# Kernel optimization log

Hardware: AMD Instinct MI355X
Metric: run time of the kernel (lower is better)

Reference implementation:

```python
import jax, jax.numpy as jnp
import numpy as np

N = 65536      # H*W pixels (256x256)
S = 1024       # superpixels
C = 128        # input channels
HIDE = 128     # hidden width
OUT = 64       # per-branch width (hide//2, concat=True)
CLS = 16       # classes
E_A = 16384    # superpixel adjacency edges
E_IMP = 6144   # importance (k=6) edges
E_PX = 1048576 # pixel row/col mask edges
EPS = 1e-5


def setup_inputs() -> dict:
    key = jax.random.key(0)
    ks = iter(jax.random.split(key, 64))
    nrm = lambda shape: jax.random.normal(next(ks), shape, dtype=jnp.float32) * 0.05
    uni = lambda shape, lo=0.0, hi=1.0: jax.random.uniform(next(ks), shape, dtype=jnp.float32, minval=lo, maxval=hi)
    ridx = lambda shape, hi: jax.random.randint(next(ks), shape, 0, hi, dtype=jnp.int32)
    d = {}
    d['x'] = jax.random.normal(next(ks), (N, C), dtype=jnp.float32)
    d['Q'] = uni((N, S))
    d['prelin_w'] = nrm((C, HIDE)); d['prelin_b'] = jnp.zeros((HIDE,), jnp.float32)
    d['bn0_g'] = jnp.ones((HIDE,), jnp.float32); d['bn0_b'] = jnp.zeros((HIDE,), jnp.float32)
    d['bn0_m'] = nrm((HIDE,)); d['bn0_v'] = uni((HIDE,), 0.5, 1.5)
    d['mmpn_w'] = nrm((5, HIDE, HIDE)); d['mmpn_b'] = jnp.zeros((5, HIDE), jnp.float32)
    d['mmpn_bn_g'] = jnp.ones((5, HIDE), jnp.float32); d['mmpn_bn_b'] = jnp.zeros((5, HIDE), jnp.float32)
    d['mmpn_bn_m'] = nrm((5, HIDE)); d['mmpn_bn_v'] = uni((5, HIDE), 0.5, 1.5)
    d['A_val'] = uni((E_A,)); d['imp_val'] = uni((E_IMP,))
    d['px_rowv_w'] = nrm((2, HIDE, OUT)); d['px_rowv_b'] = jnp.zeros((2, OUT), jnp.float32)
    d['px_colv_w'] = nrm((2, HIDE, OUT)); d['px_colv_b'] = jnp.zeros((2, OUT), jnp.float32)
    d['px_rowq_w'] = nrm((2, HIDE, OUT)); d['px_rowq_b'] = jnp.zeros((2, OUT), jnp.float32)
    d['px_colq_w'] = nrm((2, HIDE, OUT)); d['px_colq_b'] = jnp.zeros((2, OUT), jnp.float32)
    d['px_bn_g'] = jnp.ones((2, HIDE), jnp.float32); d['px_bn_b'] = jnp.zeros((2, HIDE), jnp.float32)
    d['px_bn_m'] = nrm((2, HIDE)); d['px_bn_v'] = uni((2, HIDE), 0.5, 1.5)
    d['final_w'] = nrm((HIDE, CLS)); d['final_b'] = jnp.zeros((CLS,), jnp.float32)
    d['A_src'] = ridx((E_A,), S); d['A_dst'] = ridx((E_A,), S)
    d['imp_src'] = ridx((E_IMP,), S); d['imp_dst'] = ridx((E_IMP,), S)
    d['row_src'] = ridx((E_PX,), N); d['row_dst'] = ridx((E_PX,), N)
    d['col_src'] = ridx((E_PX,), N); d['col_dst'] = ridx((E_PX,), N)
    return d


def _bn(x, g, b, m, v):
    # BatchNorm1d, eval mode (running stats)
    return g * (x - m) * jax.lax.rsqrt(v + EPS) + b


def _lrelu(x):
    return jnp.where(x >= 0, x, 0.01 * x)


def _ln(x):
    # F.layer_norm without affine params
    mu = jnp.mean(x, axis=-1, keepdims=True)
    var = jnp.mean(jnp.square(x - mu), axis=-1, keepdims=True)
    return (x - mu) * jax.lax.rsqrt(var + EPS)


def _seg_softmax(scores, ids, n):
    m = jax.ops.segment_max(scores, ids, num_segments=n)
    e = jnp.exp(scores - m[ids])
    d = jax.ops.segment_sum(e, ids, num_segments=n)
    return e / d[ids]


def _forward(x, Q, prelin_w, prelin_b, bn0_g, bn0_b, bn0_m, bn0_v,
             mmpn_w, mmpn_b, mmpn_bn_g, mmpn_bn_b, mmpn_bn_m, mmpn_bn_v,
             A_val, imp_val,
             px_rowv_w, px_rowv_b, px_colv_w, px_colv_b,
             px_rowq_w, px_rowq_b, px_colq_w, px_colq_b,
             px_bn_g, px_bn_b, px_bn_m, px_bn_v,
             final_w, final_b,
             A_src, A_dst, imp_src, imp_dst, row_src, row_dst, col_src, col_dst):
    x0 = _bn(x @ prelin_w + prelin_b, bn0_g, bn0_b, bn0_m, bn0_v)  # [N, HIDE]

    # ---- Hyperpixel_MMPN branch ----
    ncQ = Q / jnp.sum(Q, axis=0, keepdims=True)       # column-normalized Q
    hp = ncQ.T @ x0                                    # [S, HIDE]
    for i in range(5):
        h = hp @ mmpn_w[i] + mmpn_b[i]
        agg = jax.ops.segment_sum(A_val[:, None] * h[A_src], A_dst, num_segments=S)
        agg = agg + jax.ops.segment_sum(imp_val[:, None] * hp[imp_src], imp_dst, num_segments=S)
        hp = _lrelu(_bn(agg, mmpn_bn_g[i], mmpn_bn_b[i], mmpn_bn_m[i], mmpn_bn_v[i]))
    hyp = Q @ hp                                       # [N, HIDE]

    # ---- Pixel sparse-former branch ----
    px = x0
    for j in range(2):
        rowv = px @ px_rowv_w[j] + px_rowv_b[j]        # [N, OUT]
        colv = px @ px_colv_w[j] + px_colv_b[j]
        rowQ = _ln(px @ px_rowq_w[j] + px_rowq_b[j])
        colQ = _ln(px @ px_colq_w[j] + px_colq_b[j])
        rs = jnp.sum(rowQ[row_src] * rowQ[row_dst], axis=1) / OUT
        cs = jnp.sum(colQ[col_src] * colQ[col_dst], axis=1) / OUT
        ra = _seg_softmax(rs, row_src, N)
        ca = _seg_softmax(cs, col_src, N)
        rowout = jax.ops.segment_sum(rowv[row_dst] * ra[:, None], row_src, num_segments=N)
        colout = jax.ops.segment_sum(colv[col_dst] * ca[:, None], col_src, num_segments=N)
        out = jnp.concatenate((rowout, colout), axis=1)  # [N, HIDE]
        px = _lrelu(_bn(out, px_bn_g[j], px_bn_b[j], px_bn_m[j], px_bn_v[j]))

    H1 = hyp + px
    return jax.nn.softmax(H1 @ final_w + final_b, axis=-1)


def reference(x, Q, prelin_w, prelin_b, bn0_g, bn0_b, bn0_m, bn0_v,
              mmpn_w, mmpn_b, mmpn_bn_g, mmpn_bn_b, mmpn_bn_m, mmpn_bn_v,
              A_val, imp_val,
              px_rowv_w, px_rowv_b, px_colv_w, px_colv_b,
              px_rowq_w, px_rowq_b, px_colq_w, px_colq_b,
              px_bn_g, px_bn_b, px_bn_m, px_bn_v,
              final_w, final_b,
              A_src, A_dst, imp_src, imp_dst, row_src, row_dst, col_src, col_dst):
    return _forward(x, Q, prelin_w, prelin_b, bn0_g, bn0_b, bn0_m, bn0_v,
                    mmpn_w, mmpn_b, mmpn_bn_g, mmpn_bn_b, mmpn_bn_m, mmpn_bn_v,
                    A_val, imp_val,
                    px_rowv_w, px_rowv_b, px_colv_w, px_colv_b,
                    px_rowq_w, px_rowq_b, px_colq_w, px_colq_b,
                    px_bn_g, px_bn_b, px_bn_m, px_bn_v,
                    final_w, final_b,
                    A_src, A_dst, imp_src, imp_dst, row_src, row_dst, col_src, col_dst)
```

## Files before the change

kernel.cpp:

```cpp
#include <hip/hip_runtime.h>
#include <math.h>

#define N_PIX 65536
#define S_SP  1024
#define C_IN  128
#define HIDE  128
#define OUTW  64
#define NCLS  16
#define E_A   16384
#define E_IMP 6144
#define E_PX  1048576
#define EPSV  1e-5f

typedef __attribute__((ext_vector_type(4))) float f32x4;
typedef __attribute__((ext_vector_type(8))) short bf16x8;

__device__ inline ushort f2bf(float f) {
  uint u = __builtin_bit_cast(uint, f);
  uint r = (u + 0x7FFFu + ((u >> 16) & 1u)) >> 16;
  return (ushort)r;
}
__device__ inline float bf2f(uint u) {
  return __builtin_bit_cast(float, u << 16);
}

__global__ __launch_bounds__(256) void k_x0(
    const float* __restrict__ x, const float* __restrict__ W,
    const float* __restrict__ bias, const float* __restrict__ g,
    const float* __restrict__ bb, const float* __restrict__ m,
    const float* __restrict__ vv, float* __restrict__ out) {
  __shared__ float Wl[128 * 128];
  __shared__ float Xl[32 * 128];
  int t = threadIdx.x;
  int n0 = blockIdx.x * 32;
  {
    const float4* Wg = (const float4*)W;
    float4* Wd = (float4*)Wl;
#pragma unroll
    for (int i = 0; i < 16; ++i) Wd[t + 256 * i] = Wg[t + 256 * i];
    const float4* Xg = (const float4*)(x + (size_t)n0 * 128);
    float4* Xd = (float4*)Xl;
#pragma unroll
    for (int i = 0; i < 4; ++i) Xd[t + 256 * i] = Xg[t + 256 * i];
  }
  __syncthreads();
  int ht = t & 31, nt = t >> 5;
  int h0 = ht * 4, r0 = nt * 4;
  float acc[4][4];
#pragma unroll
  for (int c = 0; c < 4; ++c) {
    float bv = bias[h0 + c];
#pragma unroll
    for (int r = 0; r < 4; ++r) acc[r][c] = bv;
  }
  for (int k = 0; k < 128; k += 4) {
    float4 xr[4], wk[4];
#pragma unroll
    for (int r = 0; r < 4; ++r) xr[r] = *(const float4*)&Xl[(r0 + r) * 128 + k];
#pragma unroll
    for (int kk = 0; kk < 4; ++kk) wk[kk] = *(const float4*)&Wl[(k + kk) * 128 + h0];
#pragma unroll
    for (int r = 0; r < 4; ++r) {
      float xs[4] = {xr[r].x, xr[r].y, xr[r].z, xr[r].w};
#pragma unroll
      for (int kk = 0; kk < 4; ++kk) {
        acc[r][0] += xs[kk] * wk[kk].x;
        acc[r][1] += xs[kk] * wk[kk].y;
        acc[r][2] += xs[kk] * wk[kk].z;
        acc[r][3] += xs[kk] * wk[kk].w;
      }
    }
  }
#pragma unroll
  for (int c = 0; c < 4; ++c) {
    int h = h0 + c;
    float sc = g[h] * rsqrtf(vv[h] + EPSV);
    float mb = m[h], bo = bb[h];
#pragma unroll
    for (int r = 0; r < 4; ++r) acc[r][c] = sc * (acc[r][c] - mb) + bo;
  }
#pragma unroll
  for (int r = 0; r < 4; ++r) {
    *(float4*)&out[(size_t)(n0 + r0 + r) * 128 + h0] =
        make_float4(acc[r][0], acc[r][1], acc[r][2], acc[r][3]);
  }
}

__global__ __launch_bounds__(256) void k_cast(
    const float* __restrict__ Q, ushort* __restrict__ Qt,
    float* __restrict__ csum, ushort* __restrict__ Qbf) {
  __shared__ ushort Ot[64 * 258];
  __shared__ float Cs[64];
  int t = threadIdx.x;
  int nt = blockIdx.x & 255, st = blockIdx.x >> 8;
  int n0 = nt * 256, s0 = st * 64;
  int lr = t & 15, lg = t >> 4;
  if (t < 64) Cs[t] = 0.f;
  __syncthreads();
  float sums[4] = {0.f, 0.f, 0.f, 0.f};
#pragma unroll
  for (int nb = 0; nb < 4; ++nb) {
    ushort hh[4][4];
#pragma unroll
    for (int u = 0; u < 4; ++u) {
      int n = n0 + nb * 64 + lg * 4 + u;
      float4 q = *(const float4*)&Q[(size_t)n * 1024 + s0 + lr * 4];
      sums[0] += q.x; sums[1] += q.y; sums[2] += q.z; sums[3] += q.w;
      hh[u][0] = f2bf(q.x); hh[u][1] = f2bf(q.y);
      hh[u][2] = f2bf(q.z); hh[u][3] = f2bf(q.w);
      if (Qbf) {
        uint2 w;
        w.x = (uint)hh[u][0] | ((uint)hh[u][1] << 16);
        w.y = (uint)hh[u][2] | ((uint)hh[u][3] << 16);
        *(uint2*)&Qbf[(size_t)n * 1024 + s0 + lr * 4] = w;
      }
    }
#pragma unroll
    for (int v = 0; v < 4; ++v) {
      uint lo = (uint)hh[0][v] | ((uint)hh[1][v] << 16);
      uint hi = (uint)hh[2][v] | ((uint)hh[3][v] << 16);
      ushort* p = &Ot[(lr * 4 + v) * 258 + nb * 64 + lg * 4];
      *(uint*)p = lo;
      *(uint*)(p + 2) = hi;
    }
  }
#pragma unroll
  for (int v = 0; v < 4; ++v) atomicAdd(&Cs[lr * 4 + v], sums[v]);
  __syncthreads();
  if (t < 64) atomicAdd(&csum[s0 + t], Cs[t]);
#pragma unroll
  for (int i = 0; i < 16; ++i) {
    int v2 = i * 256 + t;
    int s_loc = v2 >> 6, nq = v2 & 63;
    const ushort* p = &Ot[s_loc * 258 + nq * 4];
    uint2 o;
    o.x = *(const uint*)p;
    o.y = *(const uint*)(p + 2);
    *(uint2*)&Qt[(size_t)(s0 + s_loc) * 65536 + n0 + nq * 4] = o;
  }
}

__global__ __launch_bounds__(256) void k_xT(
    const float* __restrict__ x0, ushort* __restrict__ x0T) {
  __shared__ ushort Ot[128 * 258];
  int t = threadIdx.x;
  int n0 = blockIdx.x * 256;
  int lr = t & 31, lg = t >> 5;
#pragma unroll
  for (int nb = 0; nb < 8; ++nb) {
    ushort hh[4][4];
#pragma unroll
    for (int u = 0; u < 4; ++u) {
      int n = n0 + nb * 32 + lg * 4 + u;
      float4 q = *(const float4*)&x0[(size_t)n * 128 + lr * 4];
      hh[u][0] = f2bf(q.x); hh[u][1] = f2bf(q.y);
      hh[u][2] = f2bf(q.z); hh[u][3] = f2bf(q.w);
    }
#pragma unroll
    for (int v = 0; v < 4; ++v) {
      uint lo = (uint)hh[0][v] | ((uint)hh[1][v] << 16);
      uint hi = (uint)hh[2][v] | ((uint)hh[3][v] << 16);
      ushort* p = &Ot[(lr * 4 + v) * 258 + nb * 32 + lg * 4];
      *(uint*)p = lo;
      *(uint*)(p + 2) = hi;
    }
  }
  __syncthreads();
#pragma unroll
  for (int i = 0; i < 32; ++i) {
    int v2 = i * 256 + t;
    int h = v2 >> 6, nq = v2 & 63;
    const ushort* p = &Ot[h * 258 + nq * 4];
    uint2 o;
    o.x = *(const uint*)p;
    o.y = *(const uint*)(p + 2);
    *(uint2*)&x0T[(size_t)h * 65536 + n0 + nq * 4] = o;
  }
}

__global__ __launch_bounds__(256) void k_hpT(
    const float* __restrict__ hp, ushort* __restrict__ hpT) {
  __shared__ ushort Ot[128 * 258];
  int t = threadIdx.x;
  int s0 = blockIdx.x * 256;
  int lr = t & 31, lg = t >> 5;
#pragma unroll
  for (int sb = 0; sb < 8; ++sb) {
    ushort hh[4][4];
#pragma unroll
    for (int u = 0; u < 4; ++u) {
      int s = s0 + sb * 32 + lg * 4 + u;
      float4 q = *(const float4*)&hp[(size_t)s * 128 + lr * 4];
      hh[u][0] = f2bf(q.x); hh[u][1] = f2bf(q.y);
      hh[u][2] = f2bf(q.z); hh[u][3] = f2bf(q.w);
    }
#pragma unroll
    for (int v = 0; v < 4; ++v) {
      uint lo = (uint)hh[0][v] | ((uint)hh[1][v] << 16);
      uint hi = (uint)hh[2][v] | ((uint)hh[3][v] << 16);
      ushort* p = &Ot[(lr * 4 + v) * 258 + sb * 32 + lg * 4];
      *(uint*)p = lo;
      *(uint*)(p + 2) = hi;
    }
  }
  __syncthreads();
#pragma unroll
  for (int i = 0; i < 32; ++i) {
    int v2 = i * 256 + t;
    int h = v2 >> 6, sq = v2 & 63;
    const ushort* p = &Ot[h * 258 + sq * 4];
    uint2 o;
    o.x = *(const uint*)p;
    o.y = *(const uint*)(p + 2);
    *(uint2*)&hpT[(size_t)h * 1024 + s0 + sq * 4] = o;
  }
}

__device__ __forceinline__ void mfma_tile128(const ushort* Al, const ushort* Bl,
                                             f32x4 acc[4][4], int wr, int wc,
                                             int lr, int lq) {
#pragma unroll
  for (int kh = 0; kh < 2; ++kh) {
    bf16x8 af[4], bf[4];
#pragma unroll
    for (int i = 0; i < 4; ++i)
      af[i] = *(const bf16x8*)&Al[(wr * 64 + i * 16 + lr) * 72 + kh * 32 + lq * 8];
#pragma unroll
    for (int j = 0; j < 4; ++j)
      bf[j] = *(const bf16x8*)&Bl[(wc * 64 + j * 16 + lr) * 72 + kh * 32 + lq * 8];
#pragma unroll
    for (int i = 0; i < 4; ++i)
#pragma unroll
      for (int j = 0; j < 4; ++j)
        acc[i][j] = __builtin_amdgcn_mfma_f32_16x16x32_bf16(af[i], bf[j],
                                                            acc[i][j], 0, 0, 0);
  }
}

__global__ __launch_bounds__(256) void k_hpu2(
    const ushort* __restrict__ Qt, const ushort* __restrict__ x0T,
    float* __restrict__ hp_part) {
  __shared__ ushort Al[2][128 * 72];
  __shared__ ushort Bl[2][128 * 72];
  int t = threadIdx.x;
  int st = blockIdx.x & 7, kb = blockIdx.x >> 3;
  int s0 = st * 128;
  int wv = t >> 6, lane = t & 63;
  int wr = wv >> 1, wc = wv & 1;
  int lr = lane & 15, lq = lane >> 4;
  int sr = t >> 3, sg = t & 7;
  const ushort* Ab = Qt + (size_t)(s0 + sr) * 65536 + (size_t)kb * 1024 + sg * 8;
  const ushort* Bb = x0T + (size_t)sr * 65536 + (size_t)kb * 1024 + sg * 8;
  f32x4 acc[4][4];
#pragma unroll
  for (int i = 0; i < 4; ++i)
#pragma unroll
    for (int j = 0; j < 4; ++j) acc[i][j] = (f32x4){0.f, 0.f, 0.f, 0.f};
  uint4 ra[4], rb[4];
#pragma unroll
  for (int i = 0; i < 4; ++i) {
    ra[i] = *(const uint4*)(Ab + (size_t)i * 32 * 65536);
    rb[i] = *(const uint4*)(Bb + (size_t)i * 32 * 65536);
  }
#pragma unroll
  for (int i = 0; i < 4; ++i) {
    *(uint4*)&Al[0][(sr + 32 * i) * 72 + sg * 8] = ra[i];
    *(uint4*)&Bl[0][(sr + 32 * i) * 72 + sg * 8] = rb[i];
  }
  __syncthreads();
  for (int c = 0; c < 16; ++c) {
    int p = c & 1;
    if (c < 15) {
      int ko = (c + 1) * 64;
#pragma unroll
      for (int i = 0; i < 4; ++i) {
        ra[i] = *(const uint4*)(Ab + (size_t)i * 32 * 65536 + ko);
        rb[i] = *(const uint4*)(Bb + (size_t)i * 32 * 65536 + ko);
      }
    }
    mfma_tile128(Al[p], Bl[p], acc, wr, wc, lr, lq);
    if (c < 15) {
      int q = p ^ 1;
#pragma unroll
      for (int i = 0; i < 4; ++i) {
        *(uint4*)&Al[q][(sr + 32 * i) * 72 + sg * 8] = ra[i];
        *(uint4*)&Bl[q][(sr + 32 * i) * 72 + sg * 8] = rb[i];
      }
    }
    __syncthreads();
  }
  float* outp = hp_part + (size_t)kb * 131072;
#pragma unroll
  for (int i = 0; i < 4; ++i) {
    int s_g = s0 + wr * 64 + i * 16 + lq * 4;
#pragma unroll
    for (int j = 0; j < 4; ++j) {
      int h = wc * 64 + j * 16 + lr;
#pragma unroll
      for (int r = 0; r < 4; ++r)
        outp[(size_t)(s_g + r) * 128 + h] = acc[i][j][r];
    }
  }
}

__global__ void k_hpred(const float* __restrict__ part,
                        const float* __restrict__ csum, float* __restrict__ hp) {
  int tid = blockIdx.x * 256 + threadIdx.x;
  float s = 0.f;
  for (int kb = 0; kb < 64; ++kb) s += part[(size_t)kb * 131072 + tid];
  hp[tid] = s / csum[tid >> 7];
}

__global__ __launch_bounds__(256) void k_hyp_bf(
    const ushort* __restrict__ Qbf, const ushort* __restrict__ hpT,
    float* __restrict__ hyp) {
  __shared__ ushort Al[2][128 * 72];
  __shared__ ushort Bl[2][128 * 72];
  int t = threadIdx.x;
  int n0 = blockIdx.x * 128;
  int wv = t >> 6, lane = t & 63;
  int wr = wv >> 1, wc = wv & 1;
  int lr = lane & 15, lq = lane >> 4;
  int sr = t >> 3, sg = t & 7;
  const ushort* Ab = Qbf + (size_t)(n0 + sr) * 1024 + sg * 8;
  const ushort* Bb = hpT + (size_t)sr * 1024 + sg * 8;
  f32x4 acc[4][4];
#pragma unroll
  for (int i = 0; i < 4; ++i)
#pragma unroll
    for (int j = 0; j < 4; ++j) acc[i][j] = (f32x4){0.f, 0.f, 0.f, 0.f};
  uint4 ra[4], rb[4];
#pragma unroll
  for (int i = 0; i < 4; ++i) {
    ra[i] = *(const uint4*)(Ab + (size_t)i * 32 * 1024);
    rb[i] = *(const uint4*)(Bb + (size_t)i * 32 * 1024);
  }
#pragma unroll
  for (int i = 0; i < 4; ++i) {
    *(uint4*)&Al[0][(sr + 32 * i) * 72 + sg * 8] = ra[i];
    *(uint4*)&Bl[0][(sr + 32 * i) * 72 + sg * 8] = rb[i];
  }
  __syncthreads();
  for (int c = 0; c < 16; ++c) {
    int p = c & 1;
    if (c < 15) {
      int ko = (c + 1) * 64;
#pragma unroll
      for (int i = 0; i < 4; ++i) {
        ra[i] = *(const uint4*)(Ab + (size_t)i * 32 * 1024 + ko);
        rb[i] = *(const uint4*)(Bb + (size_t)i * 32 * 1024 + ko);
      }
    }
    mfma_tile128(Al[p], Bl[p], acc, wr, wc, lr, lq);
    if (c < 15) {
      int q = p ^ 1;
#pragma unroll
      for (int i = 0; i < 4; ++i) {
        *(uint4*)&Al[q][(sr + 32 * i) * 72 + sg * 8] = ra[i];
        *(uint4*)&Bl[q][(sr + 32 * i) * 72 + sg * 8] = rb[i];
      }
    }
    __syncthreads();
  }
#pragma unroll
  for (int i = 0; i < 4; ++i) {
    int n_g = n0 + wr * 64 + i * 16 + lq * 4;
#pragma unroll
    for (int j = 0; j < 4; ++j) {
      int h = wc * 64 + j * 16 + lr;
#pragma unroll
      for (int r = 0; r < 4; ++r)
        hyp[(size_t)(n_g + r) * 128 + h] = acc[i][j][r];
    }
  }
}

__global__ __launch_bounds__(256) void k_hyp_f32(
    const float* __restrict__ Q, const ushort* __restrict__ hpT,
    float* __restrict__ hyp) {
  __shared__ ushort Al[2][128 * 72];
  __shared__ ushort Bl[2][128 * 72];
  int t = threadIdx.x;
  int n0 = blockIdx.x * 128;
  int wv = t >> 6, lane = t & 63;
  int wr = wv >> 1, wc = wv & 1;
  int lr = lane & 15, lq = lane >> 4;
  int ar = t >> 4, ag = t & 15;
  int sr = t >> 3, sg = t & 7;
  const float* Af = Q + (size_t)(n0 + ar) * 1024 + ag * 4;
  const ushort* Bb = hpT + (size_t)sr * 1024 + sg * 8;
  f32x4 acc[4][4];
#pragma unroll
  for (int i = 0; i < 4; ++i)
#pragma unroll
    for (int j = 0; j < 4; ++j) acc[i][j] = (f32x4){0.f, 0.f, 0.f, 0.f};
  float4 rf[8];
  uint4 rb[4];
#pragma unroll
  for (int i = 0; i < 8; ++i) rf[i] = *(const float4*)(Af + (size_t)i * 16 * 1024);
#pragma unroll
  for (int i = 0; i < 4; ++i) rb[i] = *(const uint4*)(Bb + (size_t)i * 32 * 1024);
#pragma unroll
  for (int i = 0; i < 8; ++i) {
    uint2 pk;
    pk.x = (uint)f2bf(rf[i].x) | ((uint)f2bf(rf[i].y) << 16);
    pk.y = (uint)f2bf(rf[i].z) | ((uint)f2bf(rf[i].w) << 16);
    *(uint2*)&Al[0][(ar + 16 * i) * 72 + ag * 4] = pk;
  }
#pragma unroll
  for (int i = 0; i < 4; ++i)
    *(uint4*)&Bl[0][(sr + 32 * i) * 72 + sg * 8] = rb[i];
  __syncthreads();
  for (int c = 0; c < 16; ++c) {
    int p = c & 1;
    if (c < 15) {
      int ko = (c + 1) * 64;
#pragma unroll
      for (int i = 0; i < 8; ++i)
        rf[i] = *(const float4*)(Af + (size_t)i * 16 * 1024 + ko);
#pragma unroll
      for (int i = 0; i < 4; ++i)
        rb[i] = *(const uint4*)(Bb + (size_t)i * 32 * 1024 + ko);
    }
    mfma_tile128(Al[p], Bl[p], acc, wr, wc, lr, lq);
    if (c < 15) {
      int q = p ^ 1;
#pragma unroll
      for (int i = 0; i < 8; ++i) {
        uint2 pk;
        pk.x = (uint)f2bf(rf[i].x) | ((uint)f2bf(rf[i].y) << 16);
        pk.y = (uint)f2bf(rf[i].z) | ((uint)f2bf(rf[i].w) << 16);
        *(uint2*)&Al[q][(ar + 16 * i) * 72 + ag * 4] = pk;
      }
#pragma unroll
      for (int i = 0; i < 4; ++i)
        *(uint4*)&Bl[q][(sr + 32 * i) * 72 + sg * 8] = rb[i];
    }
    __syncthreads();
  }
#pragma unroll
  for (int i = 0; i < 4; ++i) {
    int n_g = n0 + wr * 64 + i * 16 + lq * 4;
#pragma unroll
    for (int j = 0; j < 4; ++j) {
      int h = wc * 64 + j * 16 + lr;
#pragma unroll
      for (int r = 0; r < 4; ++r)
        hyp[(size_t)(n_g + r) * 128 + h] = acc[i][j][r];
    }
  }
}

__global__ __launch_bounds__(256) void k_slin(
    const float* __restrict__ A, const float* __restrict__ W,
    const float* __restrict__ bias, float* __restrict__ out) {
  __shared__ float Wl[128 * 128];
  __shared__ float Xl[32 * 128];
  int t = threadIdx.x;
  int n0 = blockIdx.x * 32;
  {
    const float4* Wg = (const float4*)W;
    float4* Wd = (float4*)Wl;
#pragma unroll
    for (int i = 0; i < 16; ++i) Wd[t + 256 * i] = Wg[t + 256 * i];
    const float4* Xg = (const float4*)(A + (size_t)n0 * 128);
    float4* Xd = (float4*)Xl;
#pragma unroll
    for (int i = 0; i < 4; ++i) Xd[t + 256 * i] = Xg[t + 256 * i];
  }
  __syncthreads();
  int ht = t & 31, nt = t >> 5;
  int h0 = ht * 4, r0 = nt * 4;
  float acc[4][4];
#pragma unroll
  for (int c = 0; c < 4; ++c) {
    float bv = bias[h0 + c];
#pragma unroll
    for (int r = 0; r < 4; ++r) acc[r][c] = bv;
  }
  for (int k = 0; k < 128; k += 4) {
    float4 xr[4], wk[4];
#pragma unroll
    for (int r = 0; r < 4; ++r) xr[r] = *(const float4*)&Xl[(r0 + r) * 128 + k];
#pragma unroll
    for (int kk = 0; kk < 4; ++kk) wk[kk] = *(const float4*)&Wl[(k + kk) * 128 + h0];
#pragma unroll
    for (int r = 0; r < 4; ++r) {
      float xs[4] = {xr[r].x, xr[r].y, xr[r].z, xr[r].w};
#pragma unroll
      for (int kk = 0; kk < 4; ++kk) {
        acc[r][0] += xs[kk] * wk[kk].x;
        acc[r][1] += xs[kk] * wk[kk].y;
        acc[r][2] += xs[kk] * wk[kk].z;
        acc[r][3] += xs[kk] * wk[kk].w;
      }
    }
  }
#pragma unroll
  for (int r = 0; r < 4; ++r) {
    *(float4*)&out[(size_t)(n0 + r0 + r) * 128 + h0] =
        make_float4(acc[r][0], acc[r][1], acc[r][2], acc[r][3]);
  }
}

__global__ __launch_bounds__(256) void k_mmpn_agg(
    const float* __restrict__ htmp, const float* __restrict__ hpin,
    const int* __restrict__ offA, const int* __restrict__ srcA,
    const float* __restrict__ valA, const int* __restrict__ offI,
    const int* __restrict__ srcI, const float* __restrict__ valI,
    const float* __restrict__ g, const float* __restrict__ b,
    const float* __restrict__ m, const float* __restrict__ v,
    float* __restrict__ hpout) {
  int s = blockIdx.x * 2 + (threadIdx.x >> 7);
  int h = threadIdx.x & 127;
  float acc = 0.f;
  int a0 = offA[s], a1 = offA[s + 1];
  for (int i = a0; i < a1; ++i)
    acc += valA[i] * htmp[(size_t)srcA[i] * 128 + h];
  int b0 = offI[s], b1 = offI[s + 1];
  for (int i = b0; i < b1; ++i)
    acc += valI[i] * hpin[(size_t)srcI[i] * 128 + h];
  float sc = g[h] * rsqrtf(v[h] + EPSV);
  float y = sc * (acc - m[h]) + b[h];
  hpout[(size_t)s * 128 + h] = y >= 0.f ? y : 0.01f * y;
}

__global__ __launch_bounds__(256) void k_pxlin(
    const float* __restrict__ px, const float* __restrict__ Wrv,
    const float* __restrict__ Wcv, const float* __restrict__ Wrq,
    const float* __restrict__ Wcq, const float* __restrict__ brv,
    const float* __restrict__ bcv, const float* __restrict__ brq,
    const float* __restrict__ bcq, float* __restrict__ out) {
  __shared__ float Xl[32 * 128];
  __shared__ float Wl[32 * 256];
  int t = threadIdx.x;
  int n0 = blockIdx.x * 32;
  {
    float4* Xd = (float4*)Xl;
    const float4* Xg = (const float4*)(px + (size_t)n0 * 128);
#pragma unroll
    for (int it = 0; it < 4; ++it) Xd[t + 256 * it] = Xg[t + 256 * it];
  }
  int ct = t & 63, nt = t >> 6;
  int c0 = ct * 4, r0 = nt * 8;
  float acc[8][4];
  {
    int mt = c0 >> 6, cb = c0 & 63;
    const float* bs = mt == 0 ? brv : mt == 1 ? bcv : mt == 2 ? brq : bcq;
#pragma unroll
    for (int c = 0; c < 4; ++c) {
      float bv = bs[cb + c];
#pragma unroll
      for (int r = 0; r < 8; ++r) acc[r][c] = bv;
    }
  }
  for (int kc = 0; kc < 4; ++kc) {
    int k0 = kc * 32;
    __syncthreads();
    {
#pragma unroll
      for (int it = 0; it < 8; ++it) {
        int v = t + 256 * it;
        int kk = v >> 6, cq = v & 63;
        int c = cq * 4;
        int mt = c >> 6, cb = c & 63;
        const float* Ws = mt == 0 ? Wrv : mt == 1 ? Wcv : mt == 2 ? Wrq : Wcq;
        *(float4*)&Wl[kk * 256 + c] = *(const float4*)&Ws[(size_t)(k0 + kk) * 64 + cb];
      }
    }
    __syncthreads();
    for (int k = 0; k < 32; k += 4) {
      float4 wq[4];
#pragma unroll
      for (int kk = 0; kk < 4; ++kk) wq[kk] = *(const float4*)&Wl[(k + kk) * 256 + c0];
#pragma unroll
      for (int r = 0; r < 8; ++r) {
        float4 xq = *(const float4*)&Xl[(r0 + r) * 128 + k0 + k];
        float xs[4] = {xq.x, xq.y, xq.z, xq.w};
#pragma unroll
        for (int kk = 0; kk < 4; ++kk) {
          acc[r][0] += xs[kk] * wq[kk].x;
          acc[r][1] += xs[kk] * wq[kk].y;
          acc[r][2] += xs[kk] * wq[kk].z;
          acc[r][3] += xs[kk] * wq[kk].w;
        }
      }
    }
  }
#pragma unroll
  for (int r = 0; r < 8; ++r) {
    *(float4*)&out[(size_t)(n0 + r0 + r) * 256 + c0] =
        make_float4(acc[r][0], acc[r][1], acc[r][2], acc[r][3]);
  }
}

__global__ __launch_bounds__(256) void k_pack(
    const float* __restrict__ lin4, uint* __restrict__ pkrow,
    uint* __restrict__ pkcol) {
  int row = blockIdx.x * 4 + (threadIdx.x >> 6);
  int l = threadIdx.x & 63;
  const float* p = lin4 + (size_t)row * 256;
#pragma unroll
  for (int gsel = 0; gsel < 2; ++gsel) {
    float q = p[128 + gsel * 64 + l];
    float s = q, s2 = q * q;
#pragma unroll
    for (int o = 32; o > 0; o >>= 1) {
      s += __shfl_xor(s, o, 64);
      s2 += __shfl_xor(s2, o, 64);
    }
    float mu = s * (1.0f / 64.0f);
    float var = s2 * (1.0f / 64.0f) - mu * mu;
    float qn = (q - mu) * rsqrtf(var + EPSV);
    float vv = p[gsel * 64 + l];
    uint pkv = (uint)f2bf(qn) | ((uint)f2bf(vv) << 16);
    (gsel ? pkcol : pkrow)[(size_t)row * 64 + l] = pkv;
  }
}

__global__ void k_hist(const int* __restrict__ src, int* __restrict__ cnt) {
  int e = blockIdx.x * 256 + threadIdx.x;
  atomicAdd(&cnt[src[e]], 1);
}

__global__ __launch_bounds__(1024) void k_scan(const int* __restrict__ cnt,
                                               int* __restrict__ off,
                                               int* __restrict__ cur) {
  __shared__ int part[1024];
  int t = threadIdx.x;
  int base = t * 64;
  int s = 0;
  for (int i = 0; i < 64; ++i) s += cnt[base + i];
  part[t] = s;
  __syncthreads();
  for (int o = 1; o < 1024; o <<= 1) {
    int v = part[t];
    int add = (t >= o) ? part[t - o] : 0;
    __syncthreads();
    part[t] = v + add;
    __syncthreads();
  }
  int run = (t > 0) ? part[t - 1] : 0;
  for (int i = 0; i < 64; ++i) {
    off[base + i] = run;
    cur[base + i] = run;
    run += cnt[base + i];
  }
  if (t == 1023) off[65536] = run;
}

__global__ __launch_bounds__(1024) void k_scan_s(const int* __restrict__ cnt,
                                                 int* __restrict__ off,
                                                 int* __restrict__ cur) {
  __shared__ int part[1024];
  int t = threadIdx.x;
  int v = cnt[t];
  part[t] = v;
  __syncthreads();
  for (int o = 1; o < 1024; o <<= 1) {
    int x = part[t];
    int a = (t >= o) ? part[t - o] : 0;
    __syncthreads();
    part[t] = x + a;
    __syncthreads();
  }
  int ex = (t > 0) ? part[t - 1] : 0;
  off[t] = ex;
  cur[t] = ex;
  if (t == 1023) off[1024] = part[1023];
}

__global__ void k_fill(const int* __restrict__ src, const int* __restrict__ dst,
                       int* __restrict__ cur, int* __restrict__ csr) {
  int e = blockIdx.x * 256 + threadIdx.x;
  int p = atomicAdd(&cur[src[e]], 1);
  csr[p] = dst[e];
}

__global__ void k_fill_v(const int* __restrict__ dst, const int* __restrict__ src,
                         const float* __restrict__ val, int* __restrict__ cur,
                         int* __restrict__ csr_src, float* __restrict__ csr_val) {
  int e = blockIdx.x * 256 + threadIdx.x;
  int p = atomicAdd(&cur[dst[e]], 1);
  csr_src[p] = src[e];
  csr_val[p] = val[e];
}

__global__ __launch_bounds__(256) void k_gather2(
    const uint* __restrict__ pk, const int* __restrict__ off,
    const int* __restrict__ csr, const float* __restrict__ g,
    const float* __restrict__ b, const float* __restrict__ m,
    const float* __restrict__ v, int ooff, float* __restrict__ outp) {
  int node = blockIdx.x * 4 + (threadIdx.x >> 6);
  int l = threadIdx.x & 63;
  uint rs = pk[(size_t)node * 64 + l];
  float qs = bf2f(rs & 0xffffu);
  int i0 = off[node], i1 = off[node + 1];
  float acc = 0.f, den = 0.f;
  int i = i0;
  for (; i + 2 <= i1; i += 2) {
    int d0 = csr[i], d1 = csr[i + 1];
    uint r0 = pk[(size_t)d0 * 64 + l];
    uint r1 = pk[(size_t)d1 * 64 + l];
    float p0 = qs * bf2f(r0 & 0xffffu);
    float p1 = qs * bf2f(r1 & 0xffffu);
#pragma unroll
    for (int o = 32; o > 0; o >>= 1) {
      p0 += __shfl_xor(p0, o, 64);
      p1 += __shfl_xor(p1, o, 64);
    }
    float w0 = __expf(p0 * (1.0f / OUTW));
    float w1 = __expf(p1 * (1.0f / OUTW));
    den += w0 + w1;
    acc += w0 * bf2f(r0 >> 16) + w1 * bf2f(r1 >> 16);
  }
  if (i < i1) {
    int d0 = csr[i];
    uint r0 = pk[(size_t)d0 * 64 + l];
    float p0 = qs * bf2f(r0 & 0xffffu);
#pragma unroll
    for (int o = 32; o > 0; o >>= 1) p0 += __shfl_xor(p0, o, 64);
    float w0 = __expf(p0 * (1.0f / OUTW));
    den += w0;
    acc += w0 * bf2f(r0 >> 16);
  }
  float r = den > 0.f ? 1.0f / den : 0.f;
  float val = acc * r;
  int h = ooff + l;
  float sc = g[h] * rsqrtf(v[h] + EPSV);
  float y = sc * (val - m[h]) + b[h];
  outp[(size_t)node * HIDE + h] = y >= 0.f ? y : 0.01f * y;
}

__global__ __launch_bounds__(256) void k_final(
    const float* __restrict__ hyp, const float* __restrict__ px,
    const float* __restrict__ W, const float* __restrict__ b,
    float* __restrict__ out) {
  __shared__ float Wl[128 * 16];
  __shared__ float rl[16 * 129];
  int t = threadIdx.x;
  int n0 = blockIdx.x * 16;
#pragma unroll
  for (int i = 0; i < 8; ++i) Wl[t + 256 * i] = W[t + 256 * i];
#pragma unroll
  for (int i = 0; i < 8; ++i) {
    int v = t + 256 * i;
    int r = v >> 7, c = v & 127;
    rl[r * 129 + c] = hyp[(size_t)(n0 + r) * 128 + c] + px[(size_t)(n0 + r) * 128 + c];
  }
  __syncthreads();
  int r = t >> 4, cls = t & 15;
  float acc = b[cls];
  for (int k = 0; k < 128; ++k) acc += rl[r * 129 + k] * Wl[k * 16 + cls];
  float mx = acc;
#pragma unroll
  for (int o = 8; o > 0; o >>= 1) mx = fmaxf(mx, __shfl_xor(mx, o, 16));
  float e = expf(acc - mx), s = e;
#pragma unroll
  for (int o = 8; o > 0; o >>= 1) s += __shfl_xor(s, o, 16);
  out[(size_t)(n0 + r) * 16 + cls] = e / s;
}

extern "C" void kernel_launch(void* const* d_in, const int* in_sizes, int n_in,
                              void* d_out, int out_size, void* d_ws, size_t ws_size,
                              hipStream_t stream) {
  const float* x        = (const float*)d_in[0];
  const float* Q        = (const float*)d_in[1];
  const float* prelin_w = (const float*)d_in[2];
  const float* prelin_b = (const float*)d_in[3];
  const float* bn0_g    = (const float*)d_in[4];
  const float* bn0_b    = (const float*)d_in[5];
  const float* bn0_m    = (const float*)d_in[6];
  const float* bn0_v    = (const float*)d_in[7];
  const float* mmpn_w   = (const float*)d_in[8];
  const float* mmpn_b   = (const float*)d_in[9];
  const float* mmpn_bn_g= (const float*)d_in[10];
  const float* mmpn_bn_b= (const float*)d_in[11];
  const float* mmpn_bn_m= (const float*)d_in[12];
  const float* mmpn_bn_v= (const float*)d_in[13];
  const float* A_val    = (const float*)d_in[14];
  const float* imp_val  = (const float*)d_in[15];
  const float* px_rowv_w= (const float*)d_in[16];
  const float* px_rowv_b= (const float*)d_in[17];
  const float* px_colv_w= (const float*)d_in[18];
  const float* px_colv_b= (const float*)d_in[19];
  const float* px_rowq_w= (const float*)d_in[20];
  const float* px_rowq_b= (const float*)d_in[21];
  const float* px_colq_w= (const float*)d_in[22];
  const float* px_colq_b= (const float*)d_in[23];
  const float* px_bn_g  = (const float*)d_in[24];
  const float* px_bn_b  = (const float*)d_in[25];
  const float* px_bn_m  = (const float*)d_in[26];
  const float* px_bn_v  = (const float*)d_in[27];
  const float* final_w  = (const float*)d_in[28];
  const float* final_b  = (const float*)d_in[29];
  const int* A_src   = (const int*)d_in[30];
  const int* A_dst   = (const int*)d_in[31];
  const int* imp_src = (const int*)d_in[32];
  const int* imp_dst = (const int*)d_in[33];
  const int* row_src = (const int*)d_in[34];
  const int* row_dst = (const int*)d_in[35];
  const int* col_src = (const int*)d_in[36];
  const int* col_dst = (const int*)d_in[37];
  float* out = (float*)d_out;

  float* ws = (float*)d_ws;
  float* x0px = ws; ws += (size_t)N_PIX * HIDE;
  float* hyp  = ws; ws += (size_t)N_PIX * HIDE;
  float* hp_part = hyp;
  float* big  = ws; ws += (size_t)32 * 1024 * 1024;
  ushort* Qt  = (ushort*)big;
  float* lin4 = big;
  int* off_row = (int*)(big + (size_t)N_PIX * 256);
  int* off_col = off_row + 65537;
  int* csr_row = off_col + 65537;
  int* csr_col = csr_row + E_PX;
  uint* pkrow = (uint*)(big + (size_t)20 * 1024 * 1024);
  uint* pkcol = pkrow + (size_t)N_PIX * 64;
  ushort* x0T = (ushort*)ws; ws += (size_t)HIDE * N_PIX / 2;
  ushort* hpT = (ushort*)ws; ws += (size_t)HIDE * S_SP / 2;
  float* csum = ws; ws += S_SP;
  float* hp   = ws; ws += (size_t)S_SP * HIDE;
  float* htmp = ws; ws += (size_t)S_SP * HIDE;
  float* agg  = ws; ws += (size_t)S_SP * HIDE;

  int* offA = (int*)ws;
  int* offI = offA + 1025;
  int* cntA = offI + 1025;
  int* cntI = cntA + 1024;
  int* curA = cntI + 1024;
  int* curI = curA + 1024;
  int* srcA = curI + 1024;
  float* valA = (float*)(srcA + E_A);
  int* srcI = (int*)(valA + E_A);
  float* valI = (float*)(srcI + E_IMP);
  ws = (float*)(valI + E_IMP);
  ws = (float*)(((uintptr_t)ws + 15) & ~(uintptr_t)15);

  size_t used = (size_t)((char*)ws - (char*)d_ws);
  ushort* Qbf = nullptr;
  if (used + (size_t)N_PIX * S_SP * sizeof(ushort) <= ws_size)
    Qbf = (ushort*)ws;

  int* cnt_row = (int*)agg;
  int* cnt_col = (int*)agg + 65536;
  int* cur_row = (int*)htmp;
  int* cur_col = (int*)htmp + 65536;

  hipMemsetAsync(csum, 0, S_SP * sizeof(float), stream);
  hipMemsetAsync(cntA, 0, 2 * 1024 * sizeof(int), stream);

  k_hist<<<E_A / 256, 256, 0, stream>>>(A_dst, cntA);
  k_hist<<<E_IMP / 256, 256, 0, stream>>>(imp_dst, cntI);
  k_scan_s<<<1, 1024, 0, stream>>>(cntA, offA, curA);
  k_scan_s<<<1, 1024, 0, stream>>>(cntI, offI, curI);
  k_fill_v<<<E_A / 256, 256, 0, stream>>>(A_dst, A_src, A_val, curA, srcA, valA);
  k_fill_v<<<E_IMP / 256, 256, 0, stream>>>(imp_dst, imp_src, imp_val, curI, srcI, valI);

  k_cast<<<4096, 256, 0, stream>>>(Q, Qt, csum, Qbf);
  k_x0<<<N_PIX / 32, 256, 0, stream>>>(x, prelin_w, prelin_b, bn0_g, bn0_b, bn0_m,
                                       bn0_v, x0px);
  k_xT<<<N_PIX / 256, 256, 0, stream>>>(x0px, x0T);
  k_hpu2<<<512, 256, 0, stream>>>(Qt, x0T, hp_part);
  k_hpred<<<S_SP * HIDE / 256, 256, 0, stream>>>(hp_part, csum, hp);

  {
    float* cur = hp;
    float* nxt = agg;
    for (int i = 0; i < 5; ++i) {
      k_slin<<<S_SP / 32, 256, 0, stream>>>(cur, mmpn_w + (size_t)i * HIDE * HIDE,
                                            mmpn_b + i * HIDE, htmp);
      k_mmpn_agg<<<S_SP / 2, 256, 0, stream>>>(
          htmp, cur, offA, srcA, valA, offI, srcI, valI,
          mmpn_bn_g + i * HIDE, mmpn_bn_b + i * HIDE, mmpn_bn_m + i * HIDE,
          mmpn_bn_v + i * HIDE, nxt);
      float* tmp = cur; cur = nxt; nxt = tmp;
    }
    k_hpT<<<S_SP / 256, 256, 0, stream>>>(cur, hpT);
  }
  if (Qbf)
    k_hyp_bf<<<N_PIX / 128, 256, 0, stream>>>(Qbf, hpT, hyp);
  else
    k_hyp_f32<<<N_PIX / 128, 256, 0, stream>>>(Q, hpT, hyp);

  hipMemsetAsync(cnt_row, 0, 2 * 65536 * sizeof(int), stream);
  k_hist<<<E_PX / 256, 256, 0, stream>>>(row_src, cnt_row);
  k_hist<<<E_PX / 256, 256, 0, stream>>>(col_src, cnt_col);
  k_scan<<<1, 1024, 0, stream>>>(cnt_row, off_row, cur_row);
  k_scan<<<1, 1024, 0, stream>>>(cnt_col, off_col, cur_col);
  k_fill<<<E_PX / 256, 256, 0, stream>>>(row_src, row_dst, cur_row, csr_row);
  k_fill<<<E_PX / 256, 256, 0, stream>>>(col_src, col_dst, cur_col, csr_col);

  for (int j = 0; j < 2; ++j) {
    k_pxlin<<<N_PIX / 32, 256, 0, stream>>>(
        x0px, px_rowv_w + j * 8192, px_colv_w + j * 8192, px_rowq_w + j * 8192,
        px_colq_w + j * 8192, px_rowv_b + j * 64, px_colv_b + j * 64,
        px_rowq_b + j * 64, px_colq_b + j * 64, lin4);
    k_pack<<<N_PIX / 4, 256, 0, stream>>>(lin4, pkrow, pkcol);
    k_gather2<<<N_PIX / 4, 256, 0, stream>>>(
        pkrow, off_row, csr_row, px_bn_g + j * HIDE, px_bn_b + j * HIDE,
        px_bn_m + j * HIDE, px_bn_v + j * HIDE, 0, x0px);
    k_gather2<<<N_PIX / 4, 256, 0, stream>>>(
        pkcol, off_col, csr_col, px_bn_g + j * HIDE, px_bn_b + j * HIDE,
        px_bn_m + j * HIDE, px_bn_v + j * HIDE, 64, x0px);
  }

  k_final<<<N_PIX / 16, 256, 0, stream>>>(hyp, x0px, final_w, final_b, out);
}
```

Before: 1.635 ms.

## Drop transposed Q copy, transpose in LDS in hpu GEMM, fuse pack into pxlin

The cast kernel now writes only a row-major bf16 copy of Q plus column sums, and no longer writes a transposed copy. The Q^T·x0 GEMM loads row-major Q and transposes it while storing to LDS, with a block remapping that groups K-chunks per XCD. Separately, the pixel linear kernel now performs the per-row layernorm and bf16 packing itself from LDS, so the lin4 intermediate and the k_pack launch go away. This saves about 128MB of writes plus one full intermediate round trip, at the cost of more complex LDS staging, strided 8-byte loads in the GEMM, and a fixed Qbf placement inside the big buffer.

Measured after the change: 1.585 ms. 3.1% less time.

```diff
diff --git a/kernel.cpp b/kernel.cpp
--- a/kernel.cpp
+++ b/kernel.cpp
@@ -86,58 +86,28 @@
   }
 }
 
-__global__ __launch_bounds__(256) void k_cast(
-    const float* __restrict__ Q, ushort* __restrict__ Qt,
-    float* __restrict__ csum, ushort* __restrict__ Qbf) {
-  __shared__ ushort Ot[64 * 258];
-  __shared__ float Cs[64];
-  int t = threadIdx.x;
-  int nt = blockIdx.x & 255, st = blockIdx.x >> 8;
-  int n0 = nt * 256, s0 = st * 64;
-  int lr = t & 15, lg = t >> 4;
-  if (t < 64) Cs[t] = 0.f;
-  __syncthreads();
-  float sums[4] = {0.f, 0.f, 0.f, 0.f};
-#pragma unroll
-  for (int nb = 0; nb < 4; ++nb) {
-    ushort hh[4][4];
-#pragma unroll
-    for (int u = 0; u < 4; ++u) {
-      int n = n0 + nb * 64 + lg * 4 + u;
-      float4 q = *(const float4*)&Q[(size_t)n * 1024 + s0 + lr * 4];
-      sums[0] += q.x; sums[1] += q.y; sums[2] += q.z; sums[3] += q.w;
-      hh[u][0] = f2bf(q.x); hh[u][1] = f2bf(q.y);
-      hh[u][2] = f2bf(q.z); hh[u][3] = f2bf(q.w);
-      if (Qbf) {
-        uint2 w;
-        w.x = (uint)hh[u][0] | ((uint)hh[u][1] << 16);
-        w.y = (uint)hh[u][2] | ((uint)hh[u][3] << 16);
-        *(uint2*)&Qbf[(size_t)n * 1024 + s0 + lr * 4] = w;
-      }
-    }
-#pragma unroll
-    for (int v = 0; v < 4; ++v) {
-      uint lo = (uint)hh[0][v] | ((uint)hh[1][v] << 16);
-      uint hi = (uint)hh[2][v] | ((uint)hh[3][v] << 16);
-      ushort* p = &Ot[(lr * 4 + v) * 258 + nb * 64 + lg * 4];
-      *(uint*)p = lo;
-      *(uint*)(p + 2) = hi;
-    }
-  }
-#pragma unroll
-  for (int v = 0; v < 4; ++v) atomicAdd(&Cs[lr * 4 + v], sums[v]);
-  __syncthreads();
-  if (t < 64) atomicAdd(&csum[s0 + t], Cs[t]);
-#pragma unroll
-  for (int i = 0; i < 16; ++i) {
-    int v2 = i * 256 + t;
-    int s_loc = v2 >> 6, nq = v2 & 63;
-    const ushort* p = &Ot[s_loc * 258 + nq * 4];
-    uint2 o;
-    o.x = *(const uint*)p;
-    o.y = *(const uint*)(p + 2);
-    *(uint2*)&Qt[(size_t)(s0 + s_loc) * 65536 + n0 + nq * 4] = o;
-  }
+__global__ __launch_bounds__(256) void k_cast2(
+    const float* __restrict__ Q, ushort* __restrict__ Qbf,
+    float* __restrict__ csum) {
+  int t = threadIdx.x;
+  int n0 = blockIdx.x * 64;
+  const float* qp = Q + (size_t)n0 * 1024 + t * 4;
+  ushort* op = Qbf + (size_t)n0 * 1024 + t * 4;
+  float s0 = 0.f, s1 = 0.f, s2 = 0.f, s3 = 0.f;
+#pragma unroll 4
+  for (int u = 0; u < 64; ++u) {
+    float4 q = *(const float4*)(qp + (size_t)u * 1024);
+    s0 += q.x; s1 += q.y; s2 += q.z; s3 += q.w;
+    uint2 w;
+    w.x = (uint)f2bf(q.x) | ((uint)f2bf(q.y) << 16);
+    w.y = (uint)f2bf(q.z) | ((uint)f2bf(q.w) << 16);
+    *(uint2*)(op + (size_t)u * 1024) = w;
+  }
+  int s = t * 4;
+  atomicAdd(&csum[s], s0);
+  atomicAdd(&csum[s + 1], s1);
+  atomicAdd(&csum[s + 2], s2);
+  atomicAdd(&csum[s + 3], s3);
 }
 
 __global__ __launch_bounds__(256) void k_xT(
@@ -237,55 +207,79 @@
   }
 }
 
-__global__ __launch_bounds__(256) void k_hpu2(
-    const ushort* __restrict__ Qt, const ushort* __restrict__ x0T,
+__device__ __forceinline__ void wrA(ushort* dst, const uint2* ra, int v) {
+  uint vals[8];
+#pragma unroll
+  for (int u = 0; u < 8; ++u) {
+    uint x = (v < 2) ? ra[u].x : ra[u].y;
+    vals[u] = (v & 1) ? (x >> 16) : (x & 0xffffu);
+  }
+  uint4 w;
+  w.x = vals[0] | (vals[1] << 16);
+  w.y = vals[2] | (vals[3] << 16);
+  w.z = vals[4] | (vals[5] << 16);
+  w.w = vals[6] | (vals[7] << 16);
+  *(uint4*)dst = w;
+}
+
+__global__ __launch_bounds__(256) void k_hpu3(
+    const ushort* __restrict__ Qbf, const ushort* __restrict__ x0T,
     float* __restrict__ hp_part) {
   __shared__ ushort Al[2][128 * 72];
   __shared__ ushort Bl[2][128 * 72];
   int t = threadIdx.x;
-  int st = blockIdx.x & 7, kb = blockIdx.x >> 3;
+  int p0 = blockIdx.x;
+  int xcd = p0 & 7, ii = p0 >> 3;
+  int kb = xcd * 8 + (ii & 7);
+  int st = ii >> 3;
   int s0 = st * 128;
+  int n_base = kb * 1024;
   int wv = t >> 6, lane = t & 63;
   int wr = wv >> 1, wc = wv & 1;
   int lr = lane & 15, lq = lane >> 4;
+  int n8 = t & 7, s4 = t >> 3;
   int sr = t >> 3, sg = t & 7;
-  const ushort* Ab = Qt + (size_t)(s0 + sr) * 65536 + (size_t)kb * 1024 + sg * 8;
-  const ushort* Bb = x0T + (size_t)sr * 65536 + (size_t)kb * 1024 + sg * 8;
+  const ushort* Ab = Qbf + (size_t)(n_base + n8 * 8) * 1024 + s0 + s4 * 4;
+  const ushort* Bb = x0T + (size_t)sr * 65536 + n_base + sg * 8;
   f32x4 acc[4][4];
 #pragma unroll
   for (int i = 0; i < 4; ++i)
 #pragma unroll
     for (int j = 0; j < 4; ++j) acc[i][j] = (f32x4){0.f, 0.f, 0.f, 0.f};
-  uint4 ra[4], rb[4];
-#pragma unroll
-  for (int i = 0; i < 4; ++i) {
-    ra[i] = *(const uint4*)(Ab + (size_t)i * 32 * 65536);
-    rb[i] = *(const uint4*)(Bb + (size_t)i * 32 * 65536);
-  }
-#pragma unroll
-  for (int i = 0; i < 4; ++i) {
-    *(uint4*)&Al[0][(sr + 32 * i) * 72 + sg * 8] = ra[i];
+  uint2 ra[8];
+  uint4 rb[4];
+#pragma unroll
+  for (int u = 0; u < 8; ++u) ra[u] = *(const uint2*)(Ab + (size_t)u * 1024);
+#pragma unroll
+  for (int i = 0; i < 4; ++i) rb[i] = *(const uint4*)(Bb + (size_t)i * 32 * 65536);
+#pragma unroll
+  for (int v = 0; v < 4; ++v)
+    wrA(&Al[0][(s4 * 4 + v) * 72 + n8 * 8], ra, v);
+#pragma unroll
+  for (int i = 0; i < 4; ++i)
     *(uint4*)&Bl[0][(sr + 32 * i) * 72 + sg * 8] = rb[i];
-  }
   __syncthreads();
   for (int c = 0; c < 16; ++c) {
     int p = c & 1;
     if (c < 15) {
-      int ko = (c + 1) * 64;
-#pragma unroll
-      for (int i = 0; i < 4; ++i) {
-        ra[i] = *(const uint4*)(Ab + (size_t)i * 32 * 65536 + ko);
-        rb[i] = *(const uint4*)(Bb + (size_t)i * 32 * 65536 + ko);
-      }
+      size_t koA = (size_t)(c + 1) * 64 * 1024;
+      int koB = (c + 1) * 64;
+#pragma unroll
+      for (int u = 0; u < 8; ++u)
+        ra[u] = *(const uint2*)(Ab + (size_t)u * 1024 + koA);
+#pragma unroll
+      for (int i = 0; i < 4; ++i)
+        rb[i] = *(const uint4*)(Bb + (size_t)i * 32 * 65536 + koB);
     }
     mfma_tile128(Al[p], Bl[p], acc, wr, wc, lr, lq);
     if (c < 15) {
       int q = p ^ 1;
 #pragma unroll
-      for (int i = 0; i < 4; ++i) {
-        *(uint4*)&Al[q][(sr + 32 * i) * 72 + sg * 8] = ra[i];
+      for (int v = 0; v < 4; ++v)
+        wrA(&Al[q][(s4 * 4 + v) * 72 + n8 * 8], ra, v);
+#pragma unroll
+      for (int i = 0; i < 4; ++i)
         *(uint4*)&Bl[q][(sr + 32 * i) * 72 + sg * 8] = rb[i];
-      }
     }
     __syncthreads();
   }
@@ -359,82 +353,6 @@
         *(uint4*)&Al[q][(sr + 32 * i) * 72 + sg * 8] = ra[i];
         *(uint4*)&Bl[q][(sr + 32 * i) * 72 + sg * 8] = rb[i];
       }
-    }
-    __syncthreads();
-  }
-#pragma unroll
-  for (int i = 0; i < 4; ++i) {
-    int n_g = n0 + wr * 64 + i * 16 + lq * 4;
-#pragma unroll
-    for (int j = 0; j < 4; ++j) {
-      int h = wc * 64 + j * 16 + lr;
-#pragma unroll
-      for (int r = 0; r < 4; ++r)
-        hyp[(size_t)(n_g + r) * 128 + h] = acc[i][j][r];
-    }
-  }
-}
-
-__global__ __launch_bounds__(256) void k_hyp_f32(
-    const float* __restrict__ Q, const ushort* __restrict__ hpT,
-    float* __restrict__ hyp) {
-  __shared__ ushort Al[2][128 * 72];
-  __shared__ ushort Bl[2][128 * 72];
-  int t = threadIdx.x;
-  int n0 = blockIdx.x * 128;
-  int wv = t >> 6, lane = t & 63;
-  int wr = wv >> 1, wc = wv & 1;
-  int lr = lane & 15, lq = lane >> 4;
-  int ar = t >> 4, ag = t & 15;
-  int sr = t >> 3, sg = t & 7;
-  const float* Af = Q + (size_t)(n0 + ar) * 1024 + ag * 4;
-  const ushort* Bb = hpT + (size_t)sr * 1024 + sg * 8;
-  f32x4 acc[4][4];
-#pragma unroll
-  for (int i = 0; i < 4; ++i)
-#pragma unroll
-    for (int j = 0; j < 4; ++j) acc[i][j] = (f32x4){0.f, 0.f, 0.f, 0.f};
-  float4 rf[8];
-  uint4 rb[4];
-#pragma unroll
-  for (int i = 0; i < 8; ++i) rf[i] = *(const float4*)(Af + (size_t)i * 16 * 1024);
-#pragma unroll
-  for (int i = 0; i < 4; ++i) rb[i] = *(const uint4*)(Bb + (size_t)i * 32 * 1024);
-#pragma unroll
-  for (int i = 0; i < 8; ++i) {
-    uint2 pk;
-    pk.x = (uint)f2bf(rf[i].x) | ((uint)f2bf(rf[i].y) << 16);
-    pk.y = (uint)f2bf(rf[i].z) | ((uint)f2bf(rf[i].w) << 16);
-    *(uint2*)&Al[0][(ar + 16 * i) * 72 + ag * 4] = pk;
-  }
-#pragma unroll
-  for (int i = 0; i < 4; ++i)
-    *(uint4*)&Bl[0][(sr + 32 * i) * 72 + sg * 8] = rb[i];
-  __syncthreads();
-  for (int c = 0; c < 16; ++c) {
-    int p = c & 1;
-    if (c < 15) {
-      int ko = (c + 1) * 64;
-#pragma unroll
-      for (int i = 0; i < 8; ++i)
-        rf[i] = *(const float4*)(Af + (size_t)i * 16 * 1024 + ko);
-#pragma unroll
-      for (int i = 0; i < 4; ++i)
-        rb[i] = *(const uint4*)(Bb + (size_t)i * 32 * 1024 + ko);
-    }
-    mfma_tile128(Al[p], Bl[p], acc, wr, wc, lr, lq);
-    if (c < 15) {
-      int q = p ^ 1;
-#pragma unroll
-      for (int i = 0; i < 8; ++i) {
-        uint2 pk;
-        pk.x = (uint)f2bf(rf[i].x) | ((uint)f2bf(rf[i].y) << 16);
-        pk.y = (uint)f2bf(rf[i].z) | ((uint)f2bf(rf[i].w) << 16);
-        *(uint2*)&Al[q][(ar + 16 * i) * 72 + ag * 4] = pk;
-      }
-#pragma unroll
-      for (int i = 0; i < 4; ++i)
-        *(uint4*)&Bl[q][(sr + 32 * i) * 72 + sg * 8] = rb[i];
     }
     __syncthreads();
   }
@@ -525,14 +443,16 @@
   hpout[(size_t)s * 128 + h] = y >= 0.f ? y : 0.01f * y;
 }
 
-__global__ __launch_bounds__(256) void k_pxlin(
+#define LP 264
+__global__ __launch_bounds__(256) void k_pxlin2(
     const float* __restrict__ px, const float* __restrict__ Wrv,
     const float* __restrict__ Wcv, const float* __restrict__ Wrq,
     const float* __restrict__ Wcq, const float* __restrict__ brv,
     const float* __restrict__ bcv, const float* __restrict__ brq,
-    const float* __restrict__ bcq, float* __restrict__ out) {
+    const float* __restrict__ bcq, uint* __restrict__ pkrow,
+    uint* __restrict__ pkcol) {
   __shared__ float Xl[32 * 128];
-  __shared__ float Wl[32 * 256];
+  __shared__ float Wl[32 * LP];
   int t = threadIdx.x;
   int n0 = blockIdx.x * 32;
   {
@@ -587,34 +507,43 @@
       }
     }
   }
-#pragma unroll
-  for (int r = 0; r < 8; ++r) {
-    *(float4*)&out[(size_t)(n0 + r0 + r) * 256 + c0] =
+  __syncthreads();
+#pragma unroll
+  for (int r = 0; r < 8; ++r)
+    *(float4*)&Wl[(r0 + r) * LP + c0] =
         make_float4(acc[r][0], acc[r][1], acc[r][2], acc[r][3]);
-  }
-}
-
-__global__ __launch_bounds__(256) void k_pack(
-    const float* __restrict__ lin4, uint* __restrict__ pkrow,
-    uint* __restrict__ pkcol) {
-  int row = blockIdx.x * 4 + (threadIdx.x >> 6);
-  int l = threadIdx.x & 63;
-  const float* p = lin4 + (size_t)row * 256;
-#pragma unroll
-  for (int gsel = 0; gsel < 2; ++gsel) {
-    float q = p[128 + gsel * 64 + l];
-    float s = q, s2 = q * q;
-#pragma unroll
-    for (int o = 32; o > 0; o >>= 1) {
+  __syncthreads();
+  int rr = t >> 3, l8 = t & 7;
+  const float* Lr = &Wl[rr * LP];
+#pragma unroll
+  for (int h = 0; h < 2; ++h) {
+    float4 qa = *(const float4*)&Lr[128 + h * 64 + l8 * 8];
+    float4 qb = *(const float4*)&Lr[128 + h * 64 + l8 * 8 + 4];
+    float s = qa.x + qa.y + qa.z + qa.w + qb.x + qb.y + qb.z + qb.w;
+    float s2 = qa.x * qa.x + qa.y * qa.y + qa.z * qa.z + qa.w * qa.w +
+               qb.x * qb.x + qb.y * qb.y + qb.z * qb.z + qb.w * qb.w;
+#pragma unroll
+    for (int o = 1; o < 8; o <<= 1) {
       s += __shfl_xor(s, o, 64);
       s2 += __shfl_xor(s2, o, 64);
     }
     float mu = s * (1.0f / 64.0f);
     float var = s2 * (1.0f / 64.0f) - mu * mu;
-    float qn = (q - mu) * rsqrtf(var + EPSV);
-    float vv = p[gsel * 64 + l];
-    uint pkv = (uint)f2bf(qn) | ((uint)f2bf(vv) << 16);
-    (gsel ? pkcol : pkrow)[(size_t)row * 64 + l] = pkv;
+    float rstd = rsqrtf(var + EPSV);
+    float4 va = *(const float4*)&Lr[h * 64 + l8 * 8];
+    float4 vb = *(const float4*)&Lr[h * 64 + l8 * 8 + 4];
+    uint4 o1, o2;
+    o1.x = (uint)f2bf((qa.x - mu) * rstd) | ((uint)f2bf(va.x) << 16);
+    o1.y = (uint)f2bf((qa.y - mu) * rstd) | ((uint)f2bf(va.y) << 16);
+    o1.z = (uint)f2bf((qa.z - mu) * rstd) | ((uint)f2bf(va.z) << 16);
+    o1.w = (uint)f2bf((qa.w - mu) * rstd) | ((uint)f2bf(va.w) << 16);
+    o2.x = (uint)f2bf((qb.x - mu) * rstd) | ((uint)f2bf(vb.x) << 16);
+    o2.y = (uint)f2bf((qb.y - mu) * rstd) | ((uint)f2bf(vb.y) << 16);
+    o2.z = (uint)f2bf((qb.z - mu) * rstd) | ((uint)f2bf(vb.z) << 16);
+    o2.w = (uint)f2bf((qb.w - mu) * rstd) | ((uint)f2bf(vb.w) << 16);
+    uint* dst = (h ? pkcol : pkrow) + (size_t)(n0 + rr) * 64 + l8 * 8;
+    *(uint4*)&dst[0] = o1;
+    *(uint4*)&dst[4] = o2;
   }
 }
 
@@ -809,8 +738,7 @@
   float* hyp  = ws; ws += (size_t)N_PIX * HIDE;
   float* hp_part = hyp;
   float* big  = ws; ws += (size_t)32 * 1024 * 1024;
-  ushort* Qt  = (ushort*)big;
-  float* lin4 = big;
+  ushort* Qbf = (ushort*)big;
   int* off_row = (int*)(big + (size_t)N_PIX * 256);
   int* off_col = off_row + 65537;
   int* csr_row = off_col + 65537;
@@ -834,13 +762,6 @@
   float* valA = (float*)(srcA + E_A);
   int* srcI = (int*)(valA + E_A);
   float* valI = (float*)(srcI + E_IMP);
-  ws = (float*)(valI + E_IMP);
-  ws = (float*)(((uintptr_t)ws + 15) & ~(uintptr_t)15);
-
-  size_t used = (size_t)((char*)ws - (char*)d_ws);
-  ushort* Qbf = nullptr;
-  if (used + (size_t)N_PIX * S_SP * sizeof(ushort) <= ws_size)
-    Qbf = (ushort*)ws;
 
   int* cnt_row = (int*)agg;
   int* cnt_col = (int*)agg + 65536;
@@ -857,11 +778,11 @@
   k_fill_v<<<E_A / 256, 256, 0, stream>>>(A_dst, A_src, A_val, curA, srcA, valA);
   k_fill_v<<<E_IMP / 256, 256, 0, stream>>>(imp_dst, imp_src, imp_val, curI, srcI, valI);
 
-  k_cast<<<4096, 256, 0, stream>>>(Q, Qt, csum, Qbf);
+  k_cast2<<<N_PIX / 64, 256, 0, stream>>>(Q, Qbf, csum);
   k_x0<<<N_PIX / 32, 256, 0, stream>>>(x, prelin_w, prelin_b, bn0_g, bn0_b, bn0_m,
                                        bn0_v, x0px);
   k_xT<<<N_PIX / 256, 256, 0, stream>>>(x0px, x0T);
-  k_hpu2<<<512, 256, 0, stream>>>(Qt, x0T, hp_part);
+  k_hpu3<<<512, 256, 0, stream>>>(Qbf, x0T, hp_part);
   k_hpred<<<S_SP * HIDE / 256, 256, 0, stream>>>(hp_part, csum, hp);
 
   {
@@ -878,10 +799,7 @@
     }
     k_hpT<<<S_SP / 256, 256, 0, stream>>>(cur, hpT);
   }
-  if (Qbf)
-    k_hyp_bf<<<N_PIX / 128, 256, 0, stream>>>(Qbf, hpT, hyp);
-  else
-    k_hyp_f32<<<N_PIX / 128, 256, 0, stream>>>(Q, hpT, hyp);
+  k_hyp_bf<<<N_PIX / 128, 256, 0, stream>>>(Qbf, hpT, hyp);
 
   hipMemsetAsync(cnt_row, 0, 2 * 65536 * sizeof(int), stream);
   k_hist<<<E_PX / 256, 256, 0, stream>>>(row_src, cnt_row);
@@ -892,11 +810,10 @@
   k_fill<<<E_PX / 256, 256, 0, stream>>>(col_src, col_dst, cur_col, csr_col);
 
   for (int j = 0; j < 2; ++j) {
-    k_pxlin<<<N_PIX / 32, 256, 0, stream>>>(
+    k_pxlin2<<<N_PIX / 32, 256, 0, stream>>>(
         x0px, px_rowv_w + j * 8192, px_colv_w + j * 8192, px_rowq_w + j * 8192,
         px_colq_w + j * 8192, px_rowv_b + j * 64, px_colv_b + j * 64,
-        px_rowq_b + j * 64, px_colq_b + j * 64, lin4);
-    k_pack<<<N_PIX / 4, 256, 0, stream>>>(lin4, pkrow, pkcol);
+        px_rowq_b + j * 64, px_colq_b + j * 64, pkrow, pkcol);
     k_gather2<<<N_PIX / 4, 256, 0, stream>>>(
         pkrow, off_row, csr_row, px_bn_g + j * HIDE, px_bn_b + j * HIDE,
         px_bn_m + j * HIDE, px_bn_v + j * HIDE, 0, x0px);
```
